# Performance work log

Measured on AMD Instinct MI355X. Metric: run time of the kernel, lower is better.

The kernel has to match this reference:

```python
import jax, jax.numpy as jnp
import numpy as np

NUM_HEADS = 12
INV_SQRT_DK = 0.125  # 1/sqrt(64)

def setup_inputs() -> dict:
    key = jax.random.key(0)
    ks = jax.random.split(key, 5)
    B, N, C = 32, 577, 768
    s = 0.02
    return {
        "x": jax.random.normal(ks[0], (B, N, C), dtype=jnp.float32),
        "W_qkv": jax.random.normal(ks[1], (C, 3 * C), dtype=jnp.float32) * s,
        "b_qkv": jax.random.normal(ks[2], (3 * C,), dtype=jnp.float32) * s,
        "W_proj": jax.random.normal(ks[3], (C, C), dtype=jnp.float32) * s,
        "b_proj": jax.random.normal(ks[4], (C,), dtype=jnp.float32) * s,
    }

def reference(x, W_qkv, b_qkv, W_proj, b_proj):
    B, N, C = x.shape
    H = NUM_HEADS
    Dh = C // H
    # qkv projection: [B,N,3C] -> [3,B,H,N,Dh]
    qkv = (x @ W_qkv + b_qkv).reshape(B, N, 3, H, Dh).transpose(2, 0, 3, 1, 4)
    q, k, v = qkv[0], qkv[1], qkv[2]
    # scaled dot-product attention, scores [B,H,N,N]
    attn = jnp.einsum("bhnd,bhmd->bhnm", q, k) * INV_SQRT_DK
    attn = jax.nn.softmax(attn, axis=-1)
    # attn_drop: rate 0 -> identity (eval)
    out = jnp.einsum("bhnm,bhmd->bhnd", attn, v)  # [B,H,N,Dh]
    out = out.transpose(0, 2, 1, 3).reshape(B, N, C)
    out = out @ W_proj + b_proj
    # proj_drop: rate 0 -> identity (eval)
    return out
```

## Files before the change

### kernel.cpp

```cpp
#include <hip/hip_runtime.h>
#include <stdint.h>

typedef __attribute__((ext_vector_type(8))) short short8;
typedef __attribute__((ext_vector_type(4))) short short4v;
typedef __attribute__((ext_vector_type(4))) float f32x4;
typedef uint2 __attribute__((aligned(2))) uint2a2;

#define MFMA(a,b,c) __builtin_amdgcn_mfma_f32_16x16x32_bf16((a),(b),(c),0,0,0)
#define QSCALE 0.18033688f
#define VT_LD 584
#define NTOK 577
#define PT_LD 72
#define AS1 __attribute__((address_space(1)))
#define AS3 __attribute__((address_space(3)))

__device__ __forceinline__ unsigned short f2bf(float f) {
    unsigned int u = __float_as_uint(f);
    u += 0x7fffu + ((u >> 16) & 1u);
    return (unsigned short)(u >> 16);
}
__device__ __forceinline__ float bf2f(unsigned short u) {
    return __uint_as_float(((unsigned int)u) << 16);
}
__device__ __forceinline__ unsigned int cvt_pk_bf16(float lo, float hi) {
    unsigned int r;
    asm("v_cvt_pk_bf16_f32 %0, %1, %2" : "=v"(r) : "v"(lo), "v"(hi));
    return r;
}

__global__ __launch_bounds__(256) void prep(
    const float* __restrict__ x, unsigned short* __restrict__ xb,
    const float* __restrict__ Wq, unsigned short* __restrict__ Wqt,
    const float* __restrict__ Wp, unsigned short* __restrict__ Wpt)
{
    __shared__ float tile[32][33];
    const int bid = blockIdx.x;
    if (bid < 13848) {
        int i = bid * 256 + threadIdx.x;
        float4 v = ((const float4*)x)[i];
        short4v s;
        s[0] = (short)f2bf(v.x); s[1] = (short)f2bf(v.y);
        s[2] = (short)f2bf(v.z); s[3] = (short)f2bf(v.w);
        ((short4v*)xb)[i] = s;
        return;
    }
    const float* in; unsigned short* out; int R, C, c0, r0;
    if (bid < 13848 + 1728) {
        int ib = bid - 13848;
        in = Wq; out = Wqt; R = 768; C = 2304;
        c0 = (ib % 72) * 32; r0 = (ib / 72) * 32;
    } else {
        int ib = bid - 15576;
        in = Wp; out = Wpt; R = 768; C = 768;
        c0 = (ib % 24) * 32; r0 = (ib / 24) * 32;
    }
    int lc = threadIdx.x & 31, lr = threadIdx.x >> 5;
    #pragma unroll
    for (int i = 0; i < 4; ++i) {
        int r = lr + i * 8;
        tile[r][lc] = in[(size_t)(r0 + r) * C + c0 + lc];
    }
    __syncthreads();
    #pragma unroll
    for (int i = 0; i < 4; ++i) {
        int r = lr + i * 8;
        out[(size_t)(c0 + r) * R + r0 + lc] = f2bf(tile[lc][r]);
    }
}

template<int EPI>
__global__ __launch_bounds__(512) void gemm256x128(
    const unsigned short* __restrict__ A,
    const unsigned short* __restrict__ Bt,
    const float* __restrict__ bias,
    unsigned short* __restrict__ q_out, unsigned short* __restrict__ k_out,
    unsigned short* __restrict__ vt_out, float* __restrict__ f_out,
    int M, int NB)
{
    __shared__ __align__(16) unsigned short As[256 * 64];
    __shared__ __align__(16) unsigned short Bs[128 * 64];

    const int nwg = gridDim.x, orig = blockIdx.x;
    const int qd = nwg >> 3, r8 = nwg & 7;
    const int xcd = orig & 7, j = orig >> 3;
    const int wg = (xcd < r8 ? xcd * (qd + 1) : r8 * (qd + 1) + (xcd - r8) * qd) + j;
    const int bx = wg % NB, by = wg / NB;
    const int m0 = by * 256, n0 = bx * 128;

    const int t = threadIdx.x, lane = t & 63, w = t >> 6;
    const int g = lane >> 4, c = lane & 15;
    const int wr = w >> 1, wcn = w & 1;
    const int srow = t >> 3;
    const int csw = (((t & 7) ^ (srow & 7)) * 8);

    f32x4 acc[4][4] = {};

    for (int k0 = 0; k0 < 768; k0 += 64) {
        #pragma unroll
        for (int i = 0; i < 4; ++i) {
            int row = i * 64 + srow;
            int ra = m0 + row; ra = ra < M ? ra : M - 1;
            __builtin_amdgcn_global_load_lds(
                (const AS1 unsigned int*)&A[(size_t)ra * 768 + k0 + csw],
                (AS3 unsigned int*)&As[i * 4096 + w * 512], 16, 0, 0);
        }
        #pragma unroll
        for (int i = 0; i < 2; ++i) {
            int row = i * 64 + srow;
            __builtin_amdgcn_global_load_lds(
                (const AS1 unsigned int*)&Bt[(size_t)(n0 + row) * 768 + k0 + csw],
                (AS3 unsigned int*)&Bs[i * 4096 + w * 512], 16, 0, 0);
        }
        __syncthreads();
        #pragma unroll
        for (int kk = 0; kk < 2; ++kk) {
            short8 af[4], bfv[4];
            #pragma unroll
            for (int mf = 0; mf < 4; ++mf) {
                int rr = wr * 64 + mf * 16 + c;
                af[mf] = *(const short8*)&As[rr * 64 + (((kk * 4 + g) ^ (c & 7)) * 8)];
            }
            #pragma unroll
            for (int nf = 0; nf < 4; ++nf) {
                int rr = wcn * 64 + nf * 16 + c;
                bfv[nf] = *(const short8*)&Bs[rr * 64 + (((kk * 4 + g) ^ (c & 7)) * 8)];
            }
            __builtin_amdgcn_s_setprio(1);
            #pragma unroll
            for (int mf = 0; mf < 4; ++mf)
            #pragma unroll
            for (int nf = 0; nf < 4; ++nf)
                acc[mf][nf] = MFMA(af[mf], bfv[nf], acc[mf][nf]);
            __builtin_amdgcn_s_setprio(0);
        }
        __syncthreads();
    }

    #pragma unroll
    for (int mf = 0; mf < 4; ++mf)
    #pragma unroll
    for (int nf = 0; nf < 4; ++nf) {
        int n = n0 + wcn * 64 + nf * 16 + c;
        float bv = bias[n];
        int mb = m0 + wr * 64 + mf * 16 + g * 4;
        if (EPI == 1) {
            #pragma unroll
            for (int e = 0; e < 4; ++e) {
                int m = mb + e;
                if (m >= M) continue;
                f_out[(size_t)m * 768 + n] = acc[mf][nf][e] + bv;
            }
        } else {
            int which = n / 768;
            int rr = n - which * 768;
            int h = rr >> 6, d = rr & 63;
            if (which == 2) {
                int b0v = mb / 577, tok0 = mb - b0v * 577;
                if (mb + 3 < M && tok0 <= 573) {
                    int bh = b0v * 12 + h;
                    uint2 pw;
                    pw.x = cvt_pk_bf16(acc[mf][nf][0] + bv, acc[mf][nf][1] + bv);
                    pw.y = cvt_pk_bf16(acc[mf][nf][2] + bv, acc[mf][nf][3] + bv);
                    *(uint2a2*)&vt_out[((size_t)bh * 64 + d) * VT_LD + tok0] = pw;
                } else {
                    #pragma unroll
                    for (int e = 0; e < 4; ++e) {
                        int m = mb + e;
                        if (m >= M) continue;
                        int b = m / 577, tok = m - b * 577;
                        vt_out[((size_t)(b * 12 + h) * 64 + d) * VT_LD + tok] =
                            f2bf(acc[mf][nf][e] + bv);
                    }
                }
            } else {
                #pragma unroll
                for (int e = 0; e < 4; ++e) {
                    int m = mb + e;
                    if (m >= M) continue;
                    int b = m / 577, tok = m - b * 577;
                    int bh = b * 12 + h;
                    if (which == 0)
                        q_out[((size_t)bh * 577 + tok) * 64 + d] = f2bf((acc[mf][nf][e] + bv) * QSCALE);
                    else
                        k_out[((size_t)bh * 577 + tok) * 64 + d] = f2bf(acc[mf][nf][e] + bv);
                }
            }
        }
    }
}

__global__ __launch_bounds__(256, 3) void attn_flash(
    const unsigned short* __restrict__ Qg,
    const unsigned short* __restrict__ Kg,
    const unsigned short* __restrict__ Vtg,
    unsigned short* __restrict__ Og)
{
    __shared__ __align__(16) unsigned short KL[2][64][64];
    __shared__ __align__(16) unsigned short VL[2][64][64];
    __shared__ __align__(16) unsigned short pt[4][16][PT_LD];

    const int nwg = gridDim.x, orig = blockIdx.x;
    const int qd = nwg >> 3, jj8 = nwg & 7;
    const int xcd = orig & 7, jj = orig >> 3;
    const int wgid = (xcd < jj8 ? xcd * (qd + 1) : jj8 * (qd + 1) + (xcd - jj8) * qd) + jj;
    const int qt = wgid % 10;
    const int bh = wgid / 10;
    const int b = bh / 12, h = bh - b * 12;
    const int t = threadIdx.x, w = t >> 6, lane = t & 63;
    const int g = lane >> 4, c = lane & 15;
    const int rowi = t >> 3;
    const int gch = ((t & 7) ^ (rowi & 7)) * 8;

    const unsigned short* Qh = Qg + (size_t)bh * NTOK * 64;
    const unsigned short* Kh = Kg + (size_t)bh * NTOK * 64;
    const unsigned short* Vh = Vtg + (size_t)bh * 64 * VT_LD;

    const int q = qt * 64 + w * 16 + c;
    const int qc = q < NTOK ? q : NTOK - 1;

    short8 bq0 = *(const short8*)&Qh[(size_t)qc * 64 +      g * 8];
    short8 bq1 = *(const short8*)&Qh[(size_t)qc * 64 + 32 + g * 8];

    auto stage = [&](int buf, int kbase) {
        #pragma unroll
        for (int i = 0; i < 2; ++i) {
            __builtin_amdgcn_global_load_lds(
                (const AS1 unsigned int*)&Kh[(size_t)(kbase + i * 32 + rowi) * 64 + gch],
                (AS3 unsigned int*)(&KL[buf][0][0] + (i * 256 + w * 64) * 8), 16, 0, 0);
            __builtin_amdgcn_global_load_lds(
                (const AS1 unsigned int*)&Vh[(size_t)(i * 32 + rowi) * VT_LD + kbase + gch],
                (AS3 unsigned int*)(&VL[buf][0][0] + (i * 256 + w * 64) * 8), 16, 0, 0);
        }
    };

    f32x4 lsumv = {};
    f32x4 ot[4] = {};

    stage(0, 0);
    __syncthreads();

    int cur = 0;
    for (int kt = 0; kt < 9; ++kt) {
        if (kt < 8) stage(cur ^ 1, (kt + 1) * 64);
        short8 kf0[4], kf1[4];
        #pragma unroll
        for (int f = 0; f < 4; ++f) {
            const unsigned short* kr = &KL[cur][f * 16 + c][0];
            kf0[f] = *(const short8*)&kr[((g    ) ^ (c & 7)) * 8];
            kf1[f] = *(const short8*)&kr[((4 + g) ^ (c & 7)) * 8];
        }
        f32x4 st[4];
        __builtin_amdgcn_s_setprio(1);
        #pragma unroll
        for (int f = 0; f < 4; ++f) {
            f32x4 z = {};
            z = MFMA(kf0[f], bq0, z);
            z = MFMA(kf1[f], bq1, z);
            st[f] = z;
        }
        __builtin_amdgcn_s_setprio(0);
        #pragma unroll
        for (int f = 0; f < 4; ++f) {
            float p0 = exp2f(fminf(st[f][0], 60.f));
            float p1 = exp2f(fminf(st[f][1], 60.f));
            float p2 = exp2f(fminf(st[f][2], 60.f));
            float p3 = exp2f(fminf(st[f][3], 60.f));
            lsumv[0] += p0; lsumv[1] += p1; lsumv[2] += p2; lsumv[3] += p3;
            uint2 pw;
            pw.x = cvt_pk_bf16(p0, p1);
            pw.y = cvt_pk_bf16(p2, p3);
            *(uint2*)&pt[w][c][f * 16 + g * 4] = pw;
        }
        __builtin_amdgcn_s_setprio(1);
        #pragma unroll
        for (int kk = 0; kk < 2; ++kk) {
            short8 bp = *(const short8*)&pt[w][c][kk * 32 + g * 8];
            #pragma unroll
            for (int df = 0; df < 4; ++df) {
                const unsigned short* vr = &VL[cur][df * 16 + c][0];
                short8 av = *(const short8*)&vr[((kk * 4 + g) ^ (c & 7)) * 8];
                ot[df] = MFMA(av, bp, ot[df]);
            }
        }
        __builtin_amdgcn_s_setprio(0);
        __syncthreads();
        cur ^= 1;
    }

    float lsum = (lsumv[0] + lsumv[1]) + (lsumv[2] + lsumv[3]);
    lsum += __shfl_xor(lsum, 16);
    lsum += __shfl_xor(lsum, 32);

    {
        const unsigned short* kp = &Kh[(size_t)576 * 64];
        float dot = 0.f;
        #pragma unroll
        for (int jx = 0; jx < 8; ++jx) {
            dot += bf2f((unsigned short)bq0[jx]) * bf2f(kp[g * 8 + jx]);
            dot += bf2f((unsigned short)bq1[jx]) * bf2f(kp[32 + g * 8 + jx]);
        }
        dot += __shfl_xor(dot, 16);
        dot += __shfl_xor(dot, 32);
        float p = exp2f(fminf(dot, 60.f));
        lsum += p;
        #pragma unroll
        for (int df = 0; df < 4; ++df)
        #pragma unroll
        for (int e = 0; e < 4; ++e)
            ot[df][e] += p * bf2f(Vh[(size_t)(df * 16 + g * 4 + e) * VT_LD + 576]);
    }

    float inv = 1.0f / lsum;
    if (q < NTOK) {
        size_t orow = ((size_t)b * NTOK + q) * 768 + h * 64;
        #pragma unroll
        for (int df = 0; df < 4; ++df) {
            uint2 ov;
            ov.x = cvt_pk_bf16(ot[df][0] * inv, ot[df][1] * inv);
            ov.y = cvt_pk_bf16(ot[df][2] * inv, ot[df][3] * inv);
            *(uint2*)&Og[orow + df * 16 + g * 4] = ov;
        }
    }
}

extern "C" void kernel_launch(void* const* d_in, const int* in_sizes, int n_in,
                              void* d_out, int out_size, void* d_ws, size_t ws_size,
                              hipStream_t stream) {
    const float* x      = (const float*)d_in[0];
    const float* W_qkv  = (const float*)d_in[1];
    const float* b_qkv  = (const float*)d_in[2];
    const float* W_proj = (const float*)d_in[3];
    const float* b_proj = (const float*)d_in[4];
    float* out = (float*)d_out;

    const int B = 32, N = 577, C = 768, H = 12;
    const int M = B * N;

    char* ws = (char*)d_ws;
    size_t off = 0;
    auto alloc = [&](size_t bytes) {
        char* p = ws + off;
        off += (bytes + 255) & ~(size_t)255;
        return p;
    };
    unsigned short* xb    = (unsigned short*)alloc((size_t)M * C * 2);
    unsigned short* wqkvt = (unsigned short*)alloc((size_t)3 * C * C * 2);
    unsigned short* wprjt = (unsigned short*)alloc((size_t)C * C * 2);
    unsigned short* Qb    = (unsigned short*)alloc((size_t)B * H * N * 64 * 2);
    unsigned short* Kb    = (unsigned short*)alloc((size_t)B * H * N * 64 * 2);
    unsigned short* Vtb   = (unsigned short*)alloc((size_t)B * H * 64 * VT_LD * 2);
    unsigned short* attn  = xb;

    prep<<<dim3(16152), 256, 0, stream>>>(x, xb, W_qkv, wqkvt, W_proj, wprjt);

    gemm256x128<0><<<dim3(73 * 18), 512, 0, stream>>>(
        xb, wqkvt, b_qkv, Qb, Kb, Vtb, nullptr, M, 18);

    attn_flash<<<dim3(3840), 256, 0, stream>>>(Qb, Kb, Vtb, attn);

    gemm256x128<1><<<dim3(73 * 6), 512, 0, stream>>>(
        attn, wprjt, b_proj, nullptr, nullptr, nullptr, out, M, 6);
}
```

Measured before the change: 210.7 us.

## Process two 64-row query tiles per attention workgroup to reuse K/V tiles

Each attention workgroup now handles 128 query rows (two 64-row sub-tiles per wave) instead of 64, so the K and V tiles staged into LDS are reused across twice as many queries and the grid is halved. This cuts global K/V traffic and staging work per query. In exchange, register pressure roughly doubles for Q fragments and accumulators, which may hurt occupancy under launch_bounds(256,3). Query rows 577..639 become padding work in the last tile. The pt scratch buffer is reused serially across the two sub-tiles.

```diff
diff --git a/kernel.cpp b/kernel.cpp
--- a/kernel.cpp
+++ b/kernel.cpp
@@ -203,8 +203,8 @@
     const int qd = nwg >> 3, jj8 = nwg & 7;
     const int xcd = orig & 7, jj = orig >> 3;
     const int wgid = (xcd < jj8 ? xcd * (qd + 1) : jj8 * (qd + 1) + (xcd - jj8) * qd) + jj;
-    const int qt = wgid % 10;
-    const int bh = wgid / 10;
+    const int qt = wgid % 5;
+    const int bh = wgid / 5;
     const int b = bh / 12, h = bh - b * 12;
     const int t = threadIdx.x, w = t >> 6, lane = t & 63;
     const int g = lane >> 4, c = lane & 15;
@@ -215,11 +215,16 @@
     const unsigned short* Kh = Kg + (size_t)bh * NTOK * 64;
     const unsigned short* Vh = Vtg + (size_t)bh * 64 * VT_LD;
 
-    const int q = qt * 64 + w * 16 + c;
-    const int qc = q < NTOK ? q : NTOK - 1;
-
-    short8 bq0 = *(const short8*)&Qh[(size_t)qc * 64 +      g * 8];
-    short8 bq1 = *(const short8*)&Qh[(size_t)qc * 64 + 32 + g * 8];
+    const int q0 = qt * 128 + w * 16 + c;
+    const int q1 = q0 + 64;
+    const int q0c = q0 < NTOK ? q0 : NTOK - 1;
+    const int q1c = q1 < NTOK ? q1 : NTOK - 1;
+
+    short8 bq[2][2];
+    bq[0][0] = *(const short8*)&Qh[(size_t)q0c * 64 +      g * 8];
+    bq[0][1] = *(const short8*)&Qh[(size_t)q0c * 64 + 32 + g * 8];
+    bq[1][0] = *(const short8*)&Qh[(size_t)q1c * 64 +      g * 8];
+    bq[1][1] = *(const short8*)&Qh[(size_t)q1c * 64 + 32 + g * 8];
 
     auto stage = [&](int buf, int kbase) {
         #pragma unroll
@@ -233,8 +238,8 @@
         }
     };
 
-    f32x4 lsumv = {};
-    f32x4 ot[4] = {};
+    f32x4 lsumv[2] = {};
+    f32x4 ot[2][4] = {};
 
     stage(0, 0);
     __syncthreads();
@@ -249,76 +254,92 @@
             kf0[f] = *(const short8*)&kr[((g    ) ^ (c & 7)) * 8];
             kf1[f] = *(const short8*)&kr[((4 + g) ^ (c & 7)) * 8];
         }
-        f32x4 st[4];
-        __builtin_amdgcn_s_setprio(1);
-        #pragma unroll
-        for (int f = 0; f < 4; ++f) {
-            f32x4 z = {};
-            z = MFMA(kf0[f], bq0, z);
-            z = MFMA(kf1[f], bq1, z);
-            st[f] = z;
-        }
-        __builtin_amdgcn_s_setprio(0);
-        #pragma unroll
-        for (int f = 0; f < 4; ++f) {
-            float p0 = exp2f(fminf(st[f][0], 60.f));
-            float p1 = exp2f(fminf(st[f][1], 60.f));
-            float p2 = exp2f(fminf(st[f][2], 60.f));
-            float p3 = exp2f(fminf(st[f][3], 60.f));
-            lsumv[0] += p0; lsumv[1] += p1; lsumv[2] += p2; lsumv[3] += p3;
-            uint2 pw;
-            pw.x = cvt_pk_bf16(p0, p1);
-            pw.y = cvt_pk_bf16(p2, p3);
-            *(uint2*)&pt[w][c][f * 16 + g * 4] = pw;
-        }
-        __builtin_amdgcn_s_setprio(1);
-        #pragma unroll
-        for (int kk = 0; kk < 2; ++kk) {
-            short8 bp = *(const short8*)&pt[w][c][kk * 32 + g * 8];
-            #pragma unroll
-            for (int df = 0; df < 4; ++df) {
-                const unsigned short* vr = &VL[cur][df * 16 + c][0];
-                short8 av = *(const short8*)&vr[((kk * 4 + g) ^ (c & 7)) * 8];
-                ot[df] = MFMA(av, bp, ot[df]);
-            }
-        }
-        __builtin_amdgcn_s_setprio(0);
+        #pragma unroll
+        for (int qq = 0; qq < 2; ++qq) {
+            f32x4 st[4];
+            __builtin_amdgcn_s_setprio(1);
+            #pragma unroll
+            for (int f = 0; f < 4; ++f) {
+                f32x4 z = {};
+                z = MFMA(kf0[f], bq[qq][0], z);
+                z = MFMA(kf1[f], bq[qq][1], z);
+                st[f] = z;
+            }
+            __builtin_amdgcn_s_setprio(0);
+            #pragma unroll
+            for (int f = 0; f < 4; ++f) {
+                float p0 = exp2f(fminf(st[f][0], 60.f));
+                float p1 = exp2f(fminf(st[f][1], 60.f));
+                float p2 = exp2f(fminf(st[f][2], 60.f));
+                float p3 = exp2f(fminf(st[f][3], 60.f));
+                lsumv[qq][0] += p0; lsumv[qq][1] += p1;
+                lsumv[qq][2] += p2; lsumv[qq][3] += p3;
+                uint2 pw;
+                pw.x = cvt_pk_bf16(p0, p1);
+                pw.y = cvt_pk_bf16(p2, p3);
+                *(uint2*)&pt[w][c][f * 16 + g * 4] = pw;
+            }
+            __builtin_amdgcn_s_setprio(1);
+            #pragma unroll
+            for (int kk = 0; kk < 2; ++kk) {
+                short8 bp = *(const short8*)&pt[w][c][kk * 32 + g * 8];
+                #pragma unroll
+                for (int df = 0; df < 4; ++df) {
+                    const unsigned short* vr = &VL[cur][df * 16 + c][0];
+                    short8 av = *(const short8*)&vr[((kk * 4 + g) ^ (c & 7)) * 8];
+                    ot[qq][df] = MFMA(av, bp, ot[qq][df]);
+                }
+            }
+            __builtin_amdgcn_s_setprio(0);
+        }
         __syncthreads();
         cur ^= 1;
     }
 
-    float lsum = (lsumv[0] + lsumv[1]) + (lsumv[2] + lsumv[3]);
-    lsum += __shfl_xor(lsum, 16);
-    lsum += __shfl_xor(lsum, 32);
+    float lsum[2];
+    #pragma unroll
+    for (int qq = 0; qq < 2; ++qq) {
+        float s = (lsumv[qq][0] + lsumv[qq][1]) + (lsumv[qq][2] + lsumv[qq][3]);
+        s += __shfl_xor(s, 16);
+        s += __shfl_xor(s, 32);
+        lsum[qq] = s;
+    }
 
     {
         const unsigned short* kp = &Kh[(size_t)576 * 64];
-        float dot = 0.f;
-        #pragma unroll
-        for (int jx = 0; jx < 8; ++jx) {
-            dot += bf2f((unsigned short)bq0[jx]) * bf2f(kp[g * 8 + jx]);
-            dot += bf2f((unsigned short)bq1[jx]) * bf2f(kp[32 + g * 8 + jx]);
-        }
-        dot += __shfl_xor(dot, 16);
-        dot += __shfl_xor(dot, 32);
-        float p = exp2f(fminf(dot, 60.f));
-        lsum += p;
-        #pragma unroll
-        for (int df = 0; df < 4; ++df)
-        #pragma unroll
-        for (int e = 0; e < 4; ++e)
-            ot[df][e] += p * bf2f(Vh[(size_t)(df * 16 + g * 4 + e) * VT_LD + 576]);
-    }
-
-    float inv = 1.0f / lsum;
-    if (q < NTOK) {
-        size_t orow = ((size_t)b * NTOK + q) * 768 + h * 64;
-        #pragma unroll
-        for (int df = 0; df < 4; ++df) {
-            uint2 ov;
-            ov.x = cvt_pk_bf16(ot[df][0] * inv, ot[df][1] * inv);
-            ov.y = cvt_pk_bf16(ot[df][2] * inv, ot[df][3] * inv);
-            *(uint2*)&Og[orow + df * 16 + g * 4] = ov;
+        #pragma unroll
+        for (int qq = 0; qq < 2; ++qq) {
+            float dot = 0.f;
+            #pragma unroll
+            for (int jx = 0; jx < 8; ++jx) {
+                dot += bf2f((unsigned short)bq[qq][0][jx]) * bf2f(kp[g * 8 + jx]);
+                dot += bf2f((unsigned short)bq[qq][1][jx]) * bf2f(kp[32 + g * 8 + jx]);
+            }
+            dot += __shfl_xor(dot, 16);
+            dot += __shfl_xor(dot, 32);
+            float p = exp2f(fminf(dot, 60.f));
+            lsum[qq] += p;
+            #pragma unroll
+            for (int df = 0; df < 4; ++df)
+            #pragma unroll
+            for (int e = 0; e < 4; ++e)
+                ot[qq][df][e] += p * bf2f(Vh[(size_t)(df * 16 + g * 4 + e) * VT_LD + 576]);
+        }
+    }
+
+    #pragma unroll
+    for (int qq = 0; qq < 2; ++qq) {
+        int q = qq == 0 ? q0 : q1;
+        if (q < NTOK) {
+            float inv = 1.0f / lsum[qq];
+            size_t orow = ((size_t)b * NTOK + q) * 768 + h * 64;
+            #pragma unroll
+            for (int df = 0; df < 4; ++df) {
+                uint2 ov;
+                ov.x = cvt_pk_bf16(ot[qq][df][0] * inv, ot[qq][df][1] * inv);
+                ov.y = cvt_pk_bf16(ot[qq][df][2] * inv, ot[qq][df][3] * inv);
+                *(uint2*)&Og[orow + df * 16 + g * 4] = ov;
+            }
         }
     }
 }
@@ -356,7 +377,7 @@
     gemm256x128<0><<<dim3(73 * 18), 512, 0, stream>>>(
         xb, wqkvt, b_qkv, Qb, Kb, Vtb, nullptr, M, 18);
 
-    attn_flash<<<dim3(3840), 256, 0, stream>>>(Qb, Kb, Vtb, attn);
+    attn_flash<<<dim3(1920), 256, 0, stream>>>(Qb, Kb, Vtb, attn);
 
     gemm256x128<1><<<dim3(73 * 6), 512, 0, stream>>>(
         attn, wprjt, b_proj, nullptr, nullptr, nullptr, out, M, 6);
```

Measured after the change: 204.7 us (median of 4 runs). 1.03x faster.
